# Performance work log

Hardware: AMD Instinct MI355X
Metric: run time of the kernel (lower is better)

## Reference

```python
import jax, jax.numpy as jnp
import numpy as np

B, S, D = 2, 2048, 2048
H, KVH = 16, 4
HD = D // H            # 128
KVD = KVH * HD         # 512
ROPE_BASE = 10000.0
EPS = 1e-6


def setup_inputs() -> dict:
    key = jax.random.key(0)
    k0, k1, k2, k3, k4, k5 = jax.random.split(key, 6)
    x = jax.random.normal(k0, (B, S, D), dtype=jnp.float32)
    # torch Linear weights are [out_features, in_features]
    Wq = jax.random.normal(k1, (D, D), dtype=jnp.float32) * 0.02
    Wk = jax.random.normal(k2, (KVD, D), dtype=jnp.float32) * 0.02
    Wv = jax.random.normal(k3, (KVD, D), dtype=jnp.float32) * 0.02
    Wproj = jax.random.normal(k4, (D, D), dtype=jnp.float32) * 0.02
    q_gain = jnp.ones((H,), dtype=jnp.float32)
    return {"x": x, "Wq": Wq, "Wk": Wk, "Wv": Wv, "Wproj": Wproj, "q_gain": q_gain}


def _rms_norm(t):
    return t * jax.lax.rsqrt(jnp.mean(t * t, axis=-1, keepdims=True) + EPS)


def _rope_tables(seqlen, dtype):
    half = HD // 2
    inv_freq = 1.0 / (ROPE_BASE ** (jnp.arange(0, HD, 2, dtype=jnp.float32) / HD))
    freqs = jnp.outer(jnp.arange(seqlen, dtype=jnp.float32), inv_freq)  # [S, half]
    return jnp.cos(freqs).astype(dtype)[None, None], jnp.sin(freqs).astype(dtype)[None, None]


def _apply_rope(t, cos, sin):
    half = t.shape[-1] // 2
    t1, t2 = t[..., :half], t[..., half:]
    return jnp.concatenate((t1 * cos + t2 * sin, -t1 * sin + t2 * cos), axis=-1)


def reference(x, Wq, Wk, Wv, Wproj, q_gain):
    bsz, seqlen, _ = x.shape
    # QKV projections (F.linear: x @ W.T)
    q = jnp.einsum('bsd,ed->bse', x, Wq).reshape(bsz, seqlen, H, HD).transpose(0, 2, 1, 3)
    k = jnp.einsum('bsd,ed->bse', x, Wk).reshape(bsz, seqlen, KVH, HD).transpose(0, 2, 1, 3)
    v = jnp.einsum('bsd,ed->bse', x, Wv).reshape(bsz, seqlen, KVH, HD).transpose(0, 2, 1, 3)
    # QK RMS-norm
    q = _rms_norm(q)
    k = _rms_norm(k)
    # RoPE
    cos, sin = _rope_tables(seqlen, q.dtype)
    q = _apply_rope(q, cos, sin)
    k = _apply_rope(k, cos, sin)
    # per-head query gain
    q = q * q_gain.astype(q.dtype)[None, :, None, None]
    # GQA: repeat_interleave kv heads
    rep = H // KVH
    k = jnp.repeat(k, rep, axis=1)
    v = jnp.repeat(v, rep, axis=1)
    # causal SDPA
    scale = 1.0 / jnp.sqrt(jnp.asarray(HD, dtype=q.dtype))
    scores = jnp.einsum('bhqd,bhkd->bhqk', q, k) * scale
    causal = jnp.tril(jnp.ones((seqlen, seqlen), dtype=bool))
    scores = jnp.where(causal[None, None], scores, jnp.finfo(scores.dtype).min)
    attn = jax.nn.softmax(scores, axis=-1)
    y = jnp.einsum('bhqk,bhkd->bhqd', attn, v)
    y = y.transpose(0, 2, 1, 3).reshape(bsz, seqlen, H * HD)
    return jnp.einsum('bse,de->bsd', y, Wproj)
```

## Files before the change

kernel.cpp:

```cpp
#include <hip/hip_runtime.h>


typedef __bf16 bf16x8 __attribute__((ext_vector_type(8)));
typedef float  f32x4  __attribute__((ext_vector_type(4)));

#define LOG2E 1.4426950408889634f
#define FIXC  16.59099297022308f

__device__ __forceinline__ float b2f(ushort h) {
  return __builtin_bit_cast(float, ((unsigned)h) << 16);
}
__device__ __forceinline__ ushort f2b(float f) {
  unsigned u = __builtin_bit_cast(unsigned, f);
  return (ushort)((u + 0x7fffu + ((u >> 16) & 1u)) >> 16);
}
__device__ __forceinline__ void async16(ushort* lds, const ushort* g) {
  __builtin_amdgcn_global_load_lds(
      (const __attribute__((address_space(1))) unsigned int*)(const void*)g,
      (__attribute__((address_space(3))) unsigned int*)(void*)lds, 16, 0, 0);
}
__device__ __forceinline__ f32x4 mfma16(bf16x8 a, bf16x8 b, f32x4 c) {
  return __builtin_amdgcn_mfma_f32_16x16x32_bf16(a, b, c, 0, 0, 0);
}

__global__ __launch_bounds__(256) void castk(const float* __restrict__ in,
                                             ushort* __restrict__ out) {
  int i = blockIdx.x * 256 + threadIdx.x;
  float4 v = ((const float4*)in)[i];
  ushort4 o = make_ushort4(f2b(v.x), f2b(v.y), f2b(v.z), f2b(v.w));
  ((ushort4*)out)[i] = o;
}

__global__ void rope_tables(float* __restrict__ cosT, float* __restrict__ sinT) {
  int s = blockIdx.x;
  int i = threadIdx.x;
  float invf = exp2f(-(float)i * (13.287712379549449f / 64.0f));
  float ang = (float)s * invf;
  float sn, cs;
  sincosf(ang, &sn, &cs);
  cosT[s * 64 + i] = cs;
  sinT[s * 64 + i] = sn;
}

__device__ __forceinline__ void store_c(float* C, size_t idx, float v) { C[idx] = v; }
__device__ __forceinline__ void store_c(ushort* C, size_t idx, float v) { C[idx] = f2b(v); }

template <typename TOUT>
__global__ __launch_bounds__(256) void gemm_bt(const ushort* __restrict__ A,
                                               const ushort* __restrict__ Bw,
                                               TOUT* __restrict__ C,
                                               int M, int N, int K) {
  __shared__ __align__(16) ushort As[128 * 32];
  __shared__ __align__(16) ushort Bs[128 * 32];
  int tid = threadIdx.x;
  int lane = tid & 63, wid = tid >> 6;
  int bm = blockIdx.y, bn = blockIdx.x;
  int wr = wid >> 1, wc = wid & 1;
  int lr = lane & 15, kg = lane >> 4;
  f32x4 z = {0.f, 0.f, 0.f, 0.f};
  f32x4 acc[4][4];
#pragma unroll
  for (int m = 0; m < 4; ++m)
#pragma unroll
    for (int n = 0; n < 4; ++n) acc[m][n] = z;

  const ushort* Ab = A + (size_t)bm * 128 * K;
  const ushort* Bb = Bw + (size_t)bn * 128 * K;
  int c0 = tid, c1 = tid + 256;

  for (int k0 = 0; k0 < K; k0 += 32) {
    async16(&As[c0 * 8], Ab + (size_t)(c0 >> 2) * K + k0 + (c0 & 3) * 8);
    async16(&As[c1 * 8], Ab + (size_t)(c1 >> 2) * K + k0 + (c1 & 3) * 8);
    async16(&Bs[c0 * 8], Bb + (size_t)(c0 >> 2) * K + k0 + (c0 & 3) * 8);
    async16(&Bs[c1 * 8], Bb + (size_t)(c1 >> 2) * K + k0 + (c1 & 3) * 8);
    __syncthreads();
    bf16x8 af[4], bfr[4];
#pragma unroll
    for (int m = 0; m < 4; ++m)
      af[m] = *(const bf16x8*)&As[(wr * 64 + m * 16 + lr) * 32 + kg * 8];
#pragma unroll
    for (int n = 0; n < 4; ++n)
      bfr[n] = *(const bf16x8*)&Bs[(wc * 64 + n * 16 + lr) * 32 + kg * 8];
#pragma unroll
    for (int m = 0; m < 4; ++m)
#pragma unroll
      for (int n = 0; n < 4; ++n)
        acc[m][n] = mfma16(af[m], bfr[n], acc[m][n]);
    __syncthreads();
  }
#pragma unroll
  for (int m = 0; m < 4; ++m)
#pragma unroll
    for (int n = 0; n < 4; ++n)
#pragma unroll
      for (int r4 = 0; r4 < 4; ++r4) {
        int row = bm * 128 + wr * 64 + m * 16 + kg * 4 + r4;
        int col = bn * 128 + wc * 64 + n * 16 + lr;
        store_c(C, (size_t)row * N + col, acc[m][n][r4]);
      }
}

__global__ __launch_bounds__(256) void rms_rope(ushort* __restrict__ qkv,
                                                const float* __restrict__ gain,
                                                const float* __restrict__ cosT,
                                                const float* __restrict__ sinT) {
  int w = blockIdx.x * 4 + (threadIdx.x >> 6);
  int lane = threadIdx.x & 63;
  int token = w / 20, slot = w % 20;
  int s = token & 2047;
  ushort* p = qkv + (size_t)token * 3072 +
              (slot < 16 ? slot * 128 : 2048 + (slot - 16) * 128);
  float t1 = b2f(p[lane]);
  float t2 = b2f(p[lane + 64]);
  float ss = t1 * t1 + t2 * t2;
#pragma unroll
  for (int off = 32; off >= 1; off >>= 1) ss += __shfl_xor(ss, off);
  float r = rsqrtf(ss * (1.0f / 128.0f) + 1e-6f);
  t1 *= r; t2 *= r;
  float c = cosT[s * 64 + lane], sn = sinT[s * 64 + lane];
  float o1 = t1 * c + t2 * sn;
  float o2 = t2 * c - t1 * sn;
  if (slot < 16) {
    float g = gain[slot] * 0.08838834764831845f;
    o1 *= g; o2 *= g;
  }
  p[lane] = f2b(o1);
  p[lane + 64] = f2b(o2);
}

__global__ __launch_bounds__(512) void attn_fwd(const ushort* __restrict__ qkv,
                                                ushort* __restrict__ y) {
  __shared__ __align__(16) ushort Qs[128 * 128];
  __shared__ __align__(16) ushort Ks[64 * 128];
  __shared__ __align__(16) ushort Vt[128 * 64];
  __shared__ __align__(16) ushort Ps[128 * 64];
  int tid = threadIdx.x, lane = tid & 63, wid = tid >> 6;
  int lr = lane & 15, kg = lane >> 4;
  int i = blockIdx.x, bh = blockIdx.y;
  int b = bh >> 4, h = bh & 15, kvh = h >> 2;
  int lo = i, hi = 31 - i;
  size_t tokbase = (size_t)b * 2048;

  bool isHi = (wid < 4);
  int wq = isHi ? wid : (wid - 4);
  int ldsrow0 = (isHi ? 0 : 64) + wq * 16;
  int qtile = isHi ? hi : lo;
  int qbase = qtile * 64 + wq * 16;

#pragma unroll
  for (int it = 0; it < 4; ++it) {
    int c = it * 512 + tid;
    int r = c >> 4, a = c & 15;
    int asrc = a ^ (r & 7);
    int qrow = (r < 64) ? hi * 64 + r : lo * 64 + (r - 64);
    async16(&Qs[c * 8], qkv + (tokbase + qrow) * 3072 + h * 128 + asrc * 8);
  }
  __syncthreads();

  bf16x8 qf[4];
#pragma unroll
  for (int kk = 0; kk < 4; ++kk) {
    int r = ldsrow0 + lr;
    int a = (kk * 4 + kg) ^ (r & 7);
    qf[kk] = *(const bf16x8*)&Qs[r * 128 + a * 8];
  }

  f32x4 z = {0.f, 0.f, 0.f, 0.f};
  f32x4 acc_y[8];
#pragma unroll
  for (int n2 = 0; n2 < 8; ++n2) acc_y[n2] = z;
  float lsum[4] = {0.f, 0.f, 0.f, 0.f};

  int nt = hi + 1;
  for (int t = 0; t < nt; ++t) {
    int kt = t * 64;
#pragma unroll
    for (int i2 = 0; i2 < 2; ++i2) {
      int c = i2 * 512 + tid;
      int r = c >> 4, a = c & 15;
      int asrc = a ^ (r & 7);
      async16(&Ks[c * 8],
              qkv + (tokbase + kt + r) * 3072 + 2048 + kvh * 128 + asrc * 8);
    }
#pragma unroll
    for (int i2 = 0; i2 < 2; ++i2) {
      int c = i2 * 512 + tid;
      int kv = c >> 4;
      int d0 = (c & 15) * 8;
      const ushort* g = qkv + (tokbase + kt + kv) * 3072 + 2560 + kvh * 128 + d0;
      union { uint4 u; ushort s[8]; } vv;
      vv.u = *(const uint4*)g;
#pragma unroll
      for (int j = 0; j < 8; ++j) {
        int d = d0 + j;
        int sw = (d & 7) ^ ((d >> 3) & 7);
        Vt[d * 64 + (kv ^ (sw << 3))] = vv.s[j];
      }
    }
    __syncthreads();

    bool act = isHi || (t <= lo);
    if (act) {
      f32x4 sc[4];
#pragma unroll
      for (int n = 0; n < 4; ++n) sc[n] = z;
      __builtin_amdgcn_s_setprio(1);
#pragma unroll
      for (int n = 0; n < 4; ++n)
#pragma unroll
        for (int kk = 0; kk < 4; ++kk) {
          int r = n * 16 + lr;
          int a = (kk * 4 + kg) ^ (r & 7);
          bf16x8 kf = *(const bf16x8*)&Ks[r * 128 + a * 8];
          sc[n] = mfma16(qf[kk], kf, sc[n]);
        }
      __builtin_amdgcn_s_setprio(0);
      if (t == qtile) {
#pragma unroll
        for (int n = 0; n < 4; ++n)
#pragma unroll
          for (int r4 = 0; r4 < 4; ++r4) {
            int kvg = kt + n * 16 + lr;
            int qg = qbase + kg * 4 + r4;
            if (kvg > qg) sc[n][r4] = -1.0e30f;
          }
      }
#pragma unroll
      for (int n = 0; n < 4; ++n)
#pragma unroll
        for (int r4 = 0; r4 < 4; ++r4) {
          float pv = __builtin_amdgcn_exp2f(fmaf(sc[n][r4], LOG2E, -FIXC));
          lsum[r4] += pv;
          int q = ldsrow0 + kg * 4 + r4;
          int col = n * 16 + lr;
          Ps[q * 64 + (col ^ ((q & 7) << 3))] = f2b(pv);
        }
      bf16x8 pa[2];
#pragma unroll
      for (int kk2 = 0; kk2 < 2; ++kk2) {
        int q = ldsrow0 + lr;
        pa[kk2] = *(const bf16x8*)&Ps[q * 64 + ((kk2 * 32 + kg * 8) ^ ((q & 7) << 3))];
      }
      __builtin_amdgcn_s_setprio(1);
#pragma unroll
      for (int n2 = 0; n2 < 8; ++n2) {
        int d = n2 * 16 + lr;
        int sw = (d & 7) ^ ((d >> 3) & 7);
#pragma unroll
        for (int kk2 = 0; kk2 < 2; ++kk2) {
          bf16x8 vb = *(const bf16x8*)&Vt[d * 64 + ((kk2 * 32 + kg * 8) ^ (sw << 3))];
          acc_y[n2] = mfma16(pa[kk2], vb, acc_y[n2]);
        }
      }
      __builtin_amdgcn_s_setprio(0);
    }
    __syncthreads();
  }

#pragma unroll
  for (int off = 1; off < 16; off <<= 1)
#pragma unroll
    for (int r4 = 0; r4 < 4; ++r4) lsum[r4] += __shfl_xor(lsum[r4], off);
  float rl[4];
#pragma unroll
  for (int r4 = 0; r4 < 4; ++r4) rl[r4] = 1.0f / lsum[r4];
#pragma unroll
  for (int n2 = 0; n2 < 8; ++n2)
#pragma unroll
    for (int r4 = 0; r4 < 4; ++r4) {
      int q = qbase + kg * 4 + r4;
      float v = acc_y[n2][r4] * rl[r4];
      y[(tokbase + q) * 2048 + h * 128 + n2 * 16 + lr] = f2b(v);
    }
}

extern "C" void kernel_launch(void* const* d_in, const int* in_sizes, int n_in,
                              void* d_out, int out_size, void* d_ws, size_t ws_size,
                              hipStream_t stream) {
  const float* x  = (const float*)d_in[0];
  const float* Wq = (const float*)d_in[1];
  const float* Wk = (const float*)d_in[2];
  const float* Wv = (const float*)d_in[3];
  const float* Wp = (const float*)d_in[4];
  const float* qg = (const float*)d_in[5];
  float* out = (float*)d_out;

  char* w = (char*)d_ws;
  ushort* xb    = (ushort*)w; w += (size_t)4096 * 2048 * 2;
  ushort* wqkv  = (ushort*)w; w += (size_t)3072 * 2048 * 2;
  ushort* wproj = (ushort*)w; w += (size_t)2048 * 2048 * 2;
  ushort* qkv   = (ushort*)w; w += (size_t)4096 * 3072 * 2;
  ushort* yb    = (ushort*)w; w += (size_t)4096 * 2048 * 2;
  float*  cosT  = (float*)w;  w += (size_t)2048 * 64 * 4;
  float*  sinT  = (float*)w;  w += (size_t)2048 * 64 * 4;

  castk<<<8192, 256, 0, stream>>>(x, xb);
  castk<<<4096, 256, 0, stream>>>(Wq, wqkv);
  castk<<<1024, 256, 0, stream>>>(Wk, wqkv + (size_t)2048 * 2048);
  castk<<<1024, 256, 0, stream>>>(Wv, wqkv + (size_t)2560 * 2048);
  castk<<<4096, 256, 0, stream>>>(Wp, wproj);
  rope_tables<<<2048, 64, 0, stream>>>(cosT, sinT);

  gemm_bt<ushort><<<dim3(24, 32), 256, 0, stream>>>(xb, wqkv, qkv, 4096, 3072, 2048);
  rms_rope<<<20480, 256, 0, stream>>>(qkv, qg, cosT, sinT);
  attn_fwd<<<dim3(16, 32), 512, 0, stream>>>(qkv, yb);
  gemm_bt<float><<<dim3(16, 32), 256, 0, stream>>>(yb, wproj, out, 4096, 2048, 2048);
}
```

Baseline: 378.6 us.

## Double-buffer K tiles and prefetch V in attention; swizzle GEMM block order

The attention kernel now keeps two K buffers in shared memory, reusing the Q staging area once Q fragments are in registers. It issues the next tile's K async loads and V register loads before computing the current tile, so global latency overlaps with the MFMA and softmax work. The GEMM kernel remaps block IDs in groups of eight to change which tiles run together, aiming at better L2 reuse across chiplets. The cost is an extra barrier, more live registers for the prefetched V, and reliance on the async K load landing before the next iteration's barrier.

```diff
diff --git a/kernel.cpp b/kernel.cpp
--- a/kernel.cpp
+++ b/kernel.cpp
@@ -54,7 +54,12 @@
   __shared__ __align__(16) ushort Bs[128 * 32];
   int tid = threadIdx.x;
   int lane = tid & 63, wid = tid >> 6;
-  int bm = blockIdx.y, bn = blockIdx.x;
+  int gx = gridDim.x;
+  int nwg = gx * gridDim.y;
+  int lid = blockIdx.y * gx + blockIdx.x;
+  int cpx = nwg >> 3;
+  int swz = (lid & 7) * cpx + (lid >> 3);
+  int bm = swz / gx, bn = swz % gx;
   int wr = wid >> 1, wc = wid & 1;
   int lr = lane & 15, kg = lane >> 4;
   f32x4 z = {0.f, 0.f, 0.f, 0.f};
@@ -130,10 +135,11 @@
 
 __global__ __launch_bounds__(512) void attn_fwd(const ushort* __restrict__ qkv,
                                                 ushort* __restrict__ y) {
-  __shared__ __align__(16) ushort Qs[128 * 128];
-  __shared__ __align__(16) ushort Ks[64 * 128];
-  __shared__ __align__(16) ushort Vt[128 * 64];
-  __shared__ __align__(16) ushort Ps[128 * 64];
+  __shared__ __align__(16) ushort LDS[32768];
+  ushort* Vt = LDS + 16384;
+  ushort* Ps = LDS + 24576;
+  ushort* Qst = LDS + 8192;
+
   int tid = threadIdx.x, lane = tid & 63, wid = tid >> 6;
   int lr = lane & 15, kg = lane >> 4;
   int i = blockIdx.x, bh = blockIdx.y;
@@ -146,6 +152,7 @@
   int ldsrow0 = (isHi ? 0 : 64) + wq * 16;
   int qtile = isHi ? hi : lo;
   int qbase = qtile * 64 + wq * 16;
+  int nt = hi + 1;
 
 #pragma unroll
   for (int it = 0; it < 4; ++it) {
@@ -153,8 +160,19 @@
     int r = c >> 4, a = c & 15;
     int asrc = a ^ (r & 7);
     int qrow = (r < 64) ? hi * 64 + r : lo * 64 + (r - 64);
-    async16(&Qs[c * 8], qkv + (tokbase + qrow) * 3072 + h * 128 + asrc * 8);
-  }
+    async16(&Qst[c * 8], qkv + (tokbase + qrow) * 3072 + h * 128 + asrc * 8);
+  }
+#pragma unroll
+  for (int i2 = 0; i2 < 2; ++i2) {
+    int c = i2 * 512 + tid;
+    int r = c >> 4, a = c & 15;
+    int asrc = a ^ (r & 7);
+    async16(&LDS[c * 8], qkv + (tokbase + r) * 3072 + 2048 + kvh * 128 + asrc * 8);
+  }
+  int vkv0 = tid >> 4, vd0 = (tid & 15) * 8;
+  uint4 va = *(const uint4*)(qkv + (tokbase + vkv0) * 3072 + 2560 + kvh * 128 + vd0);
+  uint4 vb_ = *(const uint4*)(qkv + (tokbase + 32 + vkv0) * 3072 + 2560 + kvh * 128 + vd0);
+
   __syncthreads();
 
   bf16x8 qf[4];
@@ -162,8 +180,9 @@
   for (int kk = 0; kk < 4; ++kk) {
     int r = ldsrow0 + lr;
     int a = (kk * 4 + kg) ^ (r & 7);
-    qf[kk] = *(const bf16x8*)&Qs[r * 128 + a * 8];
-  }
+    qf[kk] = *(const bf16x8*)&Qst[r * 128 + a * 8];
+  }
+  __syncthreads();
 
   f32x4 z = {0.f, 0.f, 0.f, 0.f};
   f32x4 acc_y[8];
@@ -171,36 +190,40 @@
   for (int n2 = 0; n2 < 8; ++n2) acc_y[n2] = z;
   float lsum[4] = {0.f, 0.f, 0.f, 0.f};
 
-  int nt = hi + 1;
   for (int t = 0; t < nt; ++t) {
-    int kt = t * 64;
+    ushort* kb = LDS + ((t & 1) ? 8192 : 0);
 #pragma unroll
     for (int i2 = 0; i2 < 2; ++i2) {
-      int c = i2 * 512 + tid;
-      int r = c >> 4, a = c & 15;
-      int asrc = a ^ (r & 7);
-      async16(&Ks[c * 8],
-              qkv + (tokbase + kt + r) * 3072 + 2048 + kvh * 128 + asrc * 8);
-    }
-#pragma unroll
-    for (int i2 = 0; i2 < 2; ++i2) {
-      int c = i2 * 512 + tid;
-      int kv = c >> 4;
-      int d0 = (c & 15) * 8;
-      const ushort* g = qkv + (tokbase + kt + kv) * 3072 + 2560 + kvh * 128 + d0;
       union { uint4 u; ushort s[8]; } vv;
-      vv.u = *(const uint4*)g;
+      vv.u = i2 ? vb_ : va;
+      int kv = i2 * 32 + vkv0;
 #pragma unroll
       for (int j = 0; j < 8; ++j) {
-        int d = d0 + j;
+        int d = vd0 + j;
         int sw = (d & 7) ^ ((d >> 3) & 7);
         Vt[d * 64 + (kv ^ (sw << 3))] = vv.s[j];
       }
     }
     __syncthreads();
 
+    if (t + 1 < nt) {
+      ushort* kn = LDS + (((t + 1) & 1) ? 8192 : 0);
+      int ktn = (t + 1) * 64;
+#pragma unroll
+      for (int i2 = 0; i2 < 2; ++i2) {
+        int c = i2 * 512 + tid;
+        int r = c >> 4, a = c & 15;
+        int asrc = a ^ (r & 7);
+        async16(&kn[c * 8],
+                qkv + (tokbase + ktn + r) * 3072 + 2048 + kvh * 128 + asrc * 8);
+      }
+      va  = *(const uint4*)(qkv + (tokbase + ktn + vkv0) * 3072 + 2560 + kvh * 128 + vd0);
+      vb_ = *(const uint4*)(qkv + (tokbase + ktn + 32 + vkv0) * 3072 + 2560 + kvh * 128 + vd0);
+    }
+
     bool act = isHi || (t <= lo);
     if (act) {
+      int kt = t * 64;
       f32x4 sc[4];
 #pragma unroll
       for (int n = 0; n < 4; ++n) sc[n] = z;
@@ -211,7 +234,7 @@
         for (int kk = 0; kk < 4; ++kk) {
           int r = n * 16 + lr;
           int a = (kk * 4 + kg) ^ (r & 7);
-          bf16x8 kf = *(const bf16x8*)&Ks[r * 128 + a * 8];
+          bf16x8 kf = *(const bf16x8*)&kb[r * 128 + a * 8];
           sc[n] = mfma16(qf[kk], kf, sc[n]);
         }
       __builtin_amdgcn_s_setprio(0);
```

Result: faster. 364.6 us (-3.7%).
